# Optimization experiments

Measured on AMD Instinct MI355X. Metric: run time of the kernel, lower is better.

The kernel has to match this reference:

```python
import jax, jax.numpy as jnp
import numpy as np
from jax import lax

DT = 0.01        # self.dt
DT_SCALE = 1.0   # forward default


def _christoffel(v, x, U, W):
    # Low-rank quadratic Christoffel contraction (U, W as in verlet_fused):
    # gamma = (tanh(x @ U) * (v @ U)^2) @ W        [B, D]
    h = v @ U                 # [B, R]
    gate = jnp.tanh(x @ U)    # [B, R]
    return (gate * h * h) @ W


def setup_inputs() -> dict:
    key = jax.random.key(0)
    ks = jax.random.split(key, 5)
    B, D, R = 4096, 1024, 256
    x = jax.random.normal(ks[0], (B, D), dtype=jnp.float32)
    v = jax.random.normal(ks[1], (B, D), dtype=jnp.float32)
    force = jax.random.normal(ks[2], (B, D), dtype=jnp.float32)
    U = jax.random.normal(ks[3], (D, R), dtype=jnp.float32) * (D ** -0.5)
    W = jax.random.normal(ks[4], (R, D), dtype=jnp.float32) * (R ** -0.5)
    return {"x": x, "v": v, "force": force, "U": U, "W": W, "steps": 8}


def reference(x, v, force, U, W, steps):
    dt = jnp.float32(DT * DT_SCALE)
    half = jnp.float32(0.5)

    def step(carry, _):
        x, v = carry
        a = force - _christoffel(v, x, U, W)
        v_half = v + half * dt * a
        x = x + dt * v_half
        a_next = force - _christoffel(v_half, x, U, W)
        v = v_half + half * dt * a_next
        return (x, v), None

    (x, v), _ = lax.scan(step, (x, v), None, length=steps)
    return (x, v)
```

## Files before the change

kernel.cpp:

```cpp
#include <hip/hip_runtime.h>

typedef __bf16 bf16_t;
typedef __bf16 bf16x2 __attribute__((ext_vector_type(2)));
typedef __bf16 bf16x8 __attribute__((ext_vector_type(8)));
typedef float f32x4 __attribute__((ext_vector_type(4)));

#define MFMA_BF16(a, b, c) __builtin_amdgcn_mfma_f32_16x16x32_bf16((a), (b), (c), 0, 0, 0)

static constexpr int Bn = 4096;
static constexpr int Dn = 1024;
static constexpr int Rn = 256;
static constexpr int BT = 16;
static constexpr float DTv = 0.01f;
static constexpr float HDT = 0.005f;

__global__ void pack_u_kernel(const float* __restrict__ U, bf16_t* __restrict__ Upk) {
  int t = blockIdx.x * blockDim.x + threadIdx.x;
  int l = t & 63;
  int f = t >> 6;
  int kb = f & 31;
  int ct = f >> 5;
  int row0 = kb * 32 + (l >> 4) * 8;
  int col = ct * 16 + (l & 15);
  bf16x8 v;
#pragma unroll
  for (int j = 0; j < 8; ++j) v[j] = (bf16_t)U[(size_t)(row0 + j) * Rn + col];
  ((bf16x8*)Upk)[t] = v;
}

__global__ void pack_w_kernel(const float* __restrict__ W, bf16_t* __restrict__ Wpk) {
  int t = blockIdx.x * blockDim.x + threadIdx.x;
  int l = t & 63;
  int f = t >> 6;
  int kb = f & 7;
  int ct = f >> 3;
  int row0 = kb * 32 + (l >> 4) * 8;
  int col = ct * 16 + (l & 15);
  bf16x8 v;
#pragma unroll
  for (int j = 0; j < 8; ++j) v[j] = (bf16_t)W[(size_t)(row0 + j) * Dn + col];
  ((bf16x8*)Wpk)[t] = v;
}

__global__ __launch_bounds__(1024)
void wu_mfma_kernel(const float* __restrict__ W, const bf16_t* __restrict__ Upk,
                    bf16_t* __restrict__ WUpk) {
  __shared__ __align__(16) bf16_t wbuf[16 * 1032];
  const int tid = (int)threadIdx.x;
  const int wv = tid >> 6;
  const int l = tid & 63;
  const int ln = l & 15;
  const int quad = l >> 4;
  const int m = (int)blockIdx.x;
  {
    int row = tid >> 6;
    int c0 = (tid & 63) * 16;
    const float* src = W + (size_t)(m * 16 + row) * Dn + c0;
    bf16_t* dst = wbuf + row * 1032 + c0;
#pragma unroll
    for (int j = 0; j < 16; ++j) dst[j] = (bf16_t)src[j];
  }
  __syncthreads();
  f32x4 acc = {0.f, 0.f, 0.f, 0.f};
  const bf16x8* up = (const bf16x8*)Upk + (size_t)wv * 32 * 64 + l;
  const bf16_t* arow = wbuf + ln * 1032 + quad * 8;
  bf16x8 ur[4];
#pragma unroll
  for (int p = 0; p < 4; ++p) ur[p] = up[p * 64];
#pragma unroll
  for (int kb = 0; kb < 32; ++kb) {
    const bf16x8 a = *(const bf16x8*)(arow + kb * 32);
    const bf16x8 b = ur[kb & 3];
    if (kb < 28) ur[kb & 3] = up[(kb + 4) * 64];
    acc = MFMA_BF16(a, b, acc);
  }
#pragma unroll
  for (int r = 0; r < 4; ++r) {
    int rw = m * 16 + quad * 4 + r;
    int kb = rw >> 5;
    int sub = (rw >> 3) & 3;
    int j = rw & 7;
    size_t slot = ((size_t)(wv * 8 + kb) * 64 + sub * 16 + ln) * 8 + j;
    WUpk[slot] = (bf16_t)acc[r];
  }
}

__global__ __launch_bounds__(1024)
__attribute__((amdgpu_waves_per_eu(4, 4)))
void integrate_kernel(const float* __restrict__ x_in, const float* __restrict__ v_in,
                      const float* __restrict__ force,
                      const bf16_t* __restrict__ Upk, const bf16_t* __restrict__ Wpk,
                      const bf16_t* __restrict__ WUpk,
                      const int* __restrict__ steps_p, float* __restrict__ out) {
  __shared__ __align__(16) char smem[49920];
  bf16_t* abuf = (bf16_t*)smem;
  bf16_t* tbf = (bf16_t*)smem;
  bf16_t* sbuf = (bf16_t*)smem;

  const int tid = (int)threadIdx.x;
  const int wv = tid >> 6;
  const int l = tid & 63;
  const int ln = l & 15;
  const int quad = l >> 4;
  const int s = steps_p[0];
  const int nhalf = 2 * s;
  const int row_base = (int)blockIdx.x * BT;

  float* out_x = out;
  float* out_v = out + (size_t)Bn * Dn;

  float xs[4][4], vs[4][4];
  bf16x2 fs2[4][2];

#pragma unroll
  for (int i = 0; i < 4; ++i) {
    const int col = (wv * 4 + i) * 16 + ln;
#pragma unroll
    for (int r = 0; r < 4; ++r) {
      const size_t g = (size_t)(row_base + quad * 4 + r) * Dn + col;
      xs[i][r] = x_in[g];
      vs[i][r] = v_in[g];
      fs2[i][r >> 1][r & 1] = (bf16_t)force[g];
    }
  }

  f32x4 hx = {0.f, 0.f, 0.f, 0.f};
  f32x4 hv = {0.f, 0.f, 0.f, 0.f};
  f32x4 FU = {0.f, 0.f, 0.f, 0.f};
#pragma unroll
  for (int kh = 0; kh < 2; ++kh) {
    if ((wv >> 3) == kh) {
#pragma unroll
      for (int i = 0; i < 4; ++i) {
        const int col = (wv * 4 + i) * 16 + ln - kh * 512;
#pragma unroll
        for (int r = 0; r < 4; ++r) {
          const int ro = (quad * 4 + r) * 520 + col;
          abuf[ro] = (bf16_t)xs[i][r];
          abuf[8320 + ro] = (bf16_t)vs[i][r];
          abuf[16640 + ro] = fs2[i][r >> 1][r & 1];
        }
      }
    }
    __syncthreads();
    const bf16x8* up = (const bf16x8*)Upk + ((size_t)wv * 32 + kh * 16) * 64 + l;
    const bf16_t* ax = abuf + ln * 520 + quad * 8;
    bf16x8 ur[8];
#pragma unroll
    for (int p = 0; p < 8; ++p) ur[p] = up[p * 64];
#pragma unroll
    for (int kb = 0; kb < 16; ++kb) {
      const bf16x8 b = ur[kb & 7];
      if (kb < 8) ur[kb & 7] = up[(kb + 8) * 64];
      const bf16x8 a0 = *(const bf16x8*)(ax + kb * 32);
      const bf16x8 a1 = *(const bf16x8*)(ax + 8320 + kb * 32);
      const bf16x8 a2 = *(const bf16x8*)(ax + 16640 + kb * 32);
      hx = MFMA_BF16(a0, b, hx);
      hv = MFMA_BF16(a1, b, hv);
      FU = MFMA_BF16(a2, b, FU);
    }
    __syncthreads();
  }

  bf16x8 wu[8];
  {
    const bf16x8* wub = (const bf16x8*)WUpk + (size_t)wv * 8 * 64 + l;
#pragma unroll
    for (int kb = 0; kb < 8; ++kb) wu[kb] = wub[kb * 64];
  }

  f32x4 S1 = {0.f, 0.f, 0.f, 0.f};
  f32x4 S2 = {0.f, 0.f, 0.f, 0.f};
  for (int h = 0; h < nhalf; ++h) {
    if (h & 1) {
#pragma unroll
      for (int r = 0; r < 4; ++r) hx[r] += DTv * hv[r];
    }
    const float ch = (float)(s - ((h + 1) >> 1));
#pragma unroll
    for (int r = 0; r < 4; ++r) {
      float a = fminf(fmaxf(hx[r], -15.f), 15.f);
      const float e = __expf(2.f * a);
      const float gate = (e - 1.f) / (e + 1.f);
      const float t = gate * hv[r] * hv[r];
      S1[r] += t;
      S2[r] += ch * t;
      tbf[(quad * 4 + r) * 264 + wv * 16 + ln] = (bf16_t)t;
    }
    __syncthreads();
    f32x4 g = {0.f, 0.f, 0.f, 0.f};
    const bf16_t* trow = tbf + ln * 264 + quad * 8;
#pragma unroll
    for (int kb = 0; kb < 8; ++kb) {
      const bf16x8 a = *(const bf16x8*)(trow + kb * 32);
      g = MFMA_BF16(a, wu[kb], g);
    }
#pragma unroll
    for (int r = 0; r < 4; ++r) hv[r] += HDT * (FU[r] - g[r]);
    __syncthreads();
  }

#pragma unroll
  for (int r = 0; r < 4; ++r) {
    const int ro = (quad * 4 + r) * 264 + wv * 16 + ln;
    sbuf[ro] = (bf16_t)S1[r];
    sbuf[4224 + ro] = (bf16_t)S2[r];
  }
  __syncthreads();
  f32x4 ac1[4], ac2[4];
#pragma unroll
  for (int i = 0; i < 4; ++i) {
    ac1[i] = (f32x4){0.f, 0.f, 0.f, 0.f};
    ac2[i] = (f32x4){0.f, 0.f, 0.f, 0.f};
  }
  {
    const bf16x8* wp = (const bf16x8*)Wpk + (size_t)(wv * 4) * 8 * 64 + l;
    const bf16_t* s1row = sbuf + ln * 264 + quad * 8;
    const bf16_t* s2row = s1row + 4224;
    bf16x8 wr[4];
#pragma unroll
    for (int i = 0; i < 4; ++i) wr[i] = wp[i * 8 * 64];
#pragma unroll
    for (int kb = 0; kb < 8; ++kb) {
      const bf16x8 a1 = *(const bf16x8*)(s1row + kb * 32);
      const bf16x8 a2 = *(const bf16x8*)(s2row + kb * 32);
#pragma unroll
      for (int i = 0; i < 4; ++i) {
        const bf16x8 b = wr[i];
        if (kb < 7) wr[i] = wp[i * 8 * 64 + (kb + 1) * 64];
        ac1[i] = MFMA_BF16(a1, b, ac1[i]);
        ac2[i] = MFMA_BF16(a2, b, ac2[i]);
      }
    }
  }

  const float sf = (float)s;
  const float c_vf = sf * DTv;
  const float c_xf = sf * sf * DTv * HDT;
#pragma unroll
  for (int i = 0; i < 4; ++i) {
    const int col = (wv * 4 + i) * 16 + ln;
#pragma unroll
    for (int r = 0; r < 4; ++r) {
      const size_t g = (size_t)(row_base + quad * 4 + r) * Dn + col;
      const float fv = (float)fs2[i][r >> 1][r & 1];
      out_v[g] = vs[i][r] + c_vf * fv - HDT * ac1[i][r];
      out_x[g] = xs[i][r] + c_vf * vs[i][r] + c_xf * fv - DTv * HDT * ac2[i][r];
    }
  }
}

extern "C" void kernel_launch(void* const* d_in, const int* in_sizes, int n_in,
                              void* d_out, int out_size, void* d_ws, size_t ws_size,
                              hipStream_t stream) {
  const float* x = (const float*)d_in[0];
  const float* v = (const float*)d_in[1];
  const float* force = (const float*)d_in[2];
  const float* U = (const float*)d_in[3];
  const float* W = (const float*)d_in[4];
  const int* steps = (const int*)d_in[5];

  bf16_t* Upk = (bf16_t*)d_ws;
  bf16_t* Wpk = (bf16_t*)((char*)d_ws + 512 * 1024);
  bf16_t* WUpk = (bf16_t*)((char*)d_ws + 1024 * 1024);

  pack_u_kernel<<<128, 256, 0, stream>>>(U, Upk);
  pack_w_kernel<<<128, 256, 0, stream>>>(W, Wpk);
  wu_mfma_kernel<<<16, 1024, 0, stream>>>(W, Upk, WUpk);
  integrate_kernel<<<Bn / BT, 1024, 0, stream>>>(x, v, force, Upk, Wpk, WUpk, steps,
                                                 (float*)d_out);
}
```

Measured before the change: 165.4 us.

## Merge setup kernels, stage global I/O through swizzled LDS, double-buffer step scratch

The three setup kernels (pack U, pack W, W·U product) become one launch. The WU block now reads U directly from fp32 instead of waiting on the packed copy, so one launch boundary is gone. In the integrate kernel, the loads of x, v and force and the stores of both outputs go through a swizzled shared-memory transpose, giving coalesced 16-byte global accesses in place of scattered 4-byte ones. The per-step scratch buffer is double-buffered so one barrier per half-step can be dropped, and the W·U MFMA chain is split into two accumulators. These changes add barriers around each staged I/O chunk.

```diff
diff --git a/kernel.cpp b/kernel.cpp
--- a/kernel.cpp
+++ b/kernel.cpp
@@ -14,74 +14,79 @@
 static constexpr float DTv = 0.01f;
 static constexpr float HDT = 0.005f;
 
-__global__ void pack_u_kernel(const float* __restrict__ U, bf16_t* __restrict__ Upk) {
-  int t = blockIdx.x * blockDim.x + threadIdx.x;
-  int l = t & 63;
-  int f = t >> 6;
-  int kb = f & 31;
-  int ct = f >> 5;
-  int row0 = kb * 32 + (l >> 4) * 8;
-  int col = ct * 16 + (l & 15);
-  bf16x8 v;
-#pragma unroll
-  for (int j = 0; j < 8; ++j) v[j] = (bf16_t)U[(size_t)(row0 + j) * Rn + col];
-  ((bf16x8*)Upk)[t] = v;
-}
-
-__global__ void pack_w_kernel(const float* __restrict__ W, bf16_t* __restrict__ Wpk) {
-  int t = blockIdx.x * blockDim.x + threadIdx.x;
-  int l = t & 63;
-  int f = t >> 6;
-  int kb = f & 7;
-  int ct = f >> 3;
-  int row0 = kb * 32 + (l >> 4) * 8;
-  int col = ct * 16 + (l & 15);
-  bf16x8 v;
-#pragma unroll
-  for (int j = 0; j < 8; ++j) v[j] = (bf16_t)W[(size_t)(row0 + j) * Dn + col];
-  ((bf16x8*)Wpk)[t] = v;
-}
+__device__ __forceinline__ int swz(int col) { return col ^ (((col >> 5) & 7) << 2); }
 
 __global__ __launch_bounds__(1024)
-void wu_mfma_kernel(const float* __restrict__ W, const bf16_t* __restrict__ Upk,
-                    bf16_t* __restrict__ WUpk) {
+void setup_kernel(const float* __restrict__ U, const float* __restrict__ W,
+                  bf16_t* __restrict__ Upk, bf16_t* __restrict__ Wpk,
+                  bf16_t* __restrict__ WUpk) {
   __shared__ __align__(16) bf16_t wbuf[16 * 1032];
   const int tid = (int)threadIdx.x;
-  const int wv = tid >> 6;
-  const int l = tid & 63;
-  const int ln = l & 15;
-  const int quad = l >> 4;
-  const int m = (int)blockIdx.x;
-  {
-    int row = tid >> 6;
-    int c0 = (tid & 63) * 16;
-    const float* src = W + (size_t)(m * 16 + row) * Dn + c0;
-    bf16_t* dst = wbuf + row * 1032 + c0;
-#pragma unroll
-    for (int j = 0; j < 16; ++j) dst[j] = (bf16_t)src[j];
-  }
-  __syncthreads();
-  f32x4 acc = {0.f, 0.f, 0.f, 0.f};
-  const bf16x8* up = (const bf16x8*)Upk + (size_t)wv * 32 * 64 + l;
-  const bf16_t* arow = wbuf + ln * 1032 + quad * 8;
-  bf16x8 ur[4];
-#pragma unroll
-  for (int p = 0; p < 4; ++p) ur[p] = up[p * 64];
-#pragma unroll
-  for (int kb = 0; kb < 32; ++kb) {
-    const bf16x8 a = *(const bf16x8*)(arow + kb * 32);
-    const bf16x8 b = ur[kb & 3];
-    if (kb < 28) ur[kb & 3] = up[(kb + 4) * 64];
-    acc = MFMA_BF16(a, b, acc);
-  }
-#pragma unroll
-  for (int r = 0; r < 4; ++r) {
-    int rw = m * 16 + quad * 4 + r;
-    int kb = rw >> 5;
-    int sub = (rw >> 3) & 3;
-    int j = rw & 7;
-    size_t slot = ((size_t)(wv * 8 + kb) * 64 + sub * 16 + ln) * 8 + j;
-    WUpk[slot] = (bf16_t)acc[r];
+  const int b = (int)blockIdx.x;
+  if (b < 32) {
+    int t = b * 1024 + tid;
+    int l = t & 63, f = t >> 6;
+    int kb = f & 31, ct = f >> 5;
+    int row0 = kb * 32 + (l >> 4) * 8, col = ct * 16 + (l & 15);
+    bf16x8 v;
+#pragma unroll
+    for (int j = 0; j < 8; ++j) v[j] = (bf16_t)U[(size_t)(row0 + j) * Rn + col];
+    ((bf16x8*)Upk)[t] = v;
+  } else if (b < 64) {
+    int t = (b - 32) * 1024 + tid;
+    int l = t & 63, f = t >> 6;
+    int kb = f & 7, ct = f >> 3;
+    int row0 = kb * 32 + (l >> 4) * 8, col = ct * 16 + (l & 15);
+    bf16x8 v;
+#pragma unroll
+    for (int j = 0; j < 8; ++j) v[j] = (bf16_t)W[(size_t)(row0 + j) * Dn + col];
+    ((bf16x8*)Wpk)[t] = v;
+  } else {
+    const int m = b - 64;
+    const int wv = tid >> 6;
+    const int l = tid & 63;
+    const int ln = l & 15;
+    const int quad = l >> 4;
+    {
+      int row = tid >> 6;
+      int c0 = (tid & 63) * 16;
+      const float* src = W + (size_t)(m * 16 + row) * Dn + c0;
+      bf16_t* dst = wbuf + row * 1032 + c0;
+#pragma unroll
+      for (int j = 0; j < 16; ++j) dst[j] = (bf16_t)src[j];
+    }
+    __syncthreads();
+    const int ucol = wv * 16 + ln;
+    float uf[8][8];
+#pragma unroll
+    for (int p = 0; p < 8; ++p)
+#pragma unroll
+      for (int j = 0; j < 8; ++j)
+        uf[p][j] = U[(size_t)(p * 32 + quad * 8 + j) * Rn + ucol];
+    f32x4 acc = {0.f, 0.f, 0.f, 0.f};
+    const bf16_t* arow = wbuf + ln * 1032 + quad * 8;
+#pragma unroll
+    for (int kb = 0; kb < 32; ++kb) {
+      bf16x8 bb;
+#pragma unroll
+      for (int j = 0; j < 8; ++j) bb[j] = (bf16_t)uf[kb & 7][j];
+      const bf16x8 a = *(const bf16x8*)(arow + kb * 32);
+      acc = MFMA_BF16(a, bb, acc);
+      if (kb < 24) {
+#pragma unroll
+        for (int j = 0; j < 8; ++j)
+          uf[kb & 7][j] = U[(size_t)((kb + 8) * 32 + quad * 8 + j) * Rn + ucol];
+      }
+    }
+#pragma unroll
+    for (int r = 0; r < 4; ++r) {
+      int rw = m * 16 + quad * 4 + r;
+      int kb = rw >> 5;
+      int sub = (rw >> 3) & 3;
+      int j = rw & 7;
+      size_t slot = ((size_t)(wv * 8 + kb) * 64 + sub * 16 + ln) * 8 + j;
+      WUpk[slot] = (bf16_t)acc[r];
+    }
   }
 }
 
@@ -94,8 +99,7 @@
                       const int* __restrict__ steps_p, float* __restrict__ out) {
   __shared__ __align__(16) char smem[49920];
   bf16_t* abuf = (bf16_t*)smem;
-  bf16_t* tbf = (bf16_t*)smem;
-  bf16_t* sbuf = (bf16_t*)smem;
+  float* fsb = (float*)smem;
 
   const int tid = (int)threadIdx.x;
   const int wv = tid >> 6;
@@ -109,20 +113,39 @@
   float* out_x = out;
   float* out_v = out + (size_t)Bn * Dn;
 
+  const int frow = tid >> 7;
+  const int fr = (tid & 127) * 8;
+  const int sc0 = swz(fr);
+  const int sc1 = sc0 ^ 4;
+  int csw[4];
+#pragma unroll
+  for (int i = 0; i < 4; ++i) csw[i] = swz((wv * 4 + i) * 16 + ln);
+
   float xs[4][4], vs[4][4];
   bf16x2 fs2[4][2];
 
-#pragma unroll
-  for (int i = 0; i < 4; ++i) {
-    const int col = (wv * 4 + i) * 16 + ln;
-#pragma unroll
-    for (int r = 0; r < 4; ++r) {
-      const size_t g = (size_t)(row_base + quad * 4 + r) * Dn + col;
-      xs[i][r] = x_in[g];
-      vs[i][r] = v_in[g];
-      fs2[i][r >> 1][r & 1] = (bf16_t)force[g];
-    }
-  }
+  auto load_chunk = [&](const float* __restrict__ srcA, int HF, auto sink) {
+    const float* src_ = srcA + (size_t)(row_base + HF * 8) * Dn;
+    f32x4 a_ = *(const f32x4*)(src_ + tid * 8);
+    f32x4 b_ = *(const f32x4*)(src_ + tid * 8 + 4);
+    *(f32x4*)(fsb + frow * 1024 + sc0) = a_;
+    *(f32x4*)(fsb + frow * 1024 + sc1) = b_;
+    __syncthreads();
+    if ((quad >> 1) == HF) {
+#pragma unroll
+      for (int i = 0; i < 4; ++i)
+#pragma unroll
+        for (int r = 0; r < 4; ++r)
+          sink(i, r, fsb[((quad & 1) * 4 + r) * 1024 + csw[i]]);
+    }
+    __syncthreads();
+  };
+  load_chunk(x_in, 0, [&](int i, int r, float v_) { xs[i][r] = v_; });
+  load_chunk(x_in, 1, [&](int i, int r, float v_) { xs[i][r] = v_; });
+  load_chunk(v_in, 0, [&](int i, int r, float v_) { vs[i][r] = v_; });
+  load_chunk(v_in, 1, [&](int i, int r, float v_) { vs[i][r] = v_; });
+  load_chunk(force, 0, [&](int i, int r, float v_) { fs2[i][r >> 1][r & 1] = (bf16_t)v_; });
+  load_chunk(force, 1, [&](int i, int r, float v_) { fs2[i][r >> 1][r & 1] = (bf16_t)v_; });
 
   f32x4 hx = {0.f, 0.f, 0.f, 0.f};
   f32x4 hv = {0.f, 0.f, 0.f, 0.f};
@@ -171,12 +194,14 @@
 
   f32x4 S1 = {0.f, 0.f, 0.f, 0.f};
   f32x4 S2 = {0.f, 0.f, 0.f, 0.f};
+  bf16_t* tbase = (bf16_t*)smem;
   for (int h = 0; h < nhalf; ++h) {
     if (h & 1) {
 #pragma unroll
       for (int r = 0; r < 4; ++r) hx[r] += DTv * hv[r];
     }
     const float ch = (float)(s - ((h + 1) >> 1));
+    bf16_t* tb = tbase + (h & 1) * 4224;
 #pragma unroll
     for (int r = 0; r < 4; ++r) {
       float a = fminf(fmaxf(hx[r], -15.f), 15.f);
@@ -185,21 +210,23 @@
       const float t = gate * hv[r] * hv[r];
       S1[r] += t;
       S2[r] += ch * t;
-      tbf[(quad * 4 + r) * 264 + wv * 16 + ln] = (bf16_t)t;
-    }
-    __syncthreads();
-    f32x4 g = {0.f, 0.f, 0.f, 0.f};
-    const bf16_t* trow = tbf + ln * 264 + quad * 8;
-#pragma unroll
-    for (int kb = 0; kb < 8; ++kb) {
-      const bf16x8 a = *(const bf16x8*)(trow + kb * 32);
-      g = MFMA_BF16(a, wu[kb], g);
-    }
-#pragma unroll
-    for (int r = 0; r < 4; ++r) hv[r] += HDT * (FU[r] - g[r]);
-    __syncthreads();
-  }
-
+      tb[(quad * 4 + r) * 264 + wv * 16 + ln] = (bf16_t)t;
+    }
+    __syncthreads();
+    f32x4 g0 = {0.f, 0.f, 0.f, 0.f};
+    f32x4 g1 = {0.f, 0.f, 0.f, 0.f};
+    const bf16_t* trow = tb + ln * 264 + quad * 8;
+#pragma unroll
+    for (int kb = 0; kb < 8; kb += 2) {
+      g0 = MFMA_BF16(*(const bf16x8*)(trow + kb * 32), wu[kb], g0);
+      g1 = MFMA_BF16(*(const bf16x8*)(trow + (kb + 1) * 32), wu[kb + 1], g1);
+    }
+#pragma unroll
+    for (int r = 0; r < 4; ++r) hv[r] += HDT * (FU[r] - (g0[r] + g1[r]));
+  }
+  __syncthreads();
+
+  bf16_t* sbuf = (bf16_t*)smem;
 #pragma unroll
   for (int r = 0; r < 4; ++r) {
     const int ro = (quad * 4 + r) * 264 + wv * 16 + ln;
@@ -233,21 +260,36 @@
       }
     }
   }
+  __syncthreads();
 
   const float sf = (float)s;
   const float c_vf = sf * DTv;
   const float c_xf = sf * sf * DTv * HDT;
-#pragma unroll
-  for (int i = 0; i < 4; ++i) {
-    const int col = (wv * 4 + i) * 16 + ln;
-#pragma unroll
-    for (int r = 0; r < 4; ++r) {
-      const size_t g = (size_t)(row_base + quad * 4 + r) * Dn + col;
-      const float fv = (float)fs2[i][r >> 1][r & 1];
-      out_v[g] = vs[i][r] + c_vf * fv - HDT * ac1[i][r];
-      out_x[g] = xs[i][r] + c_vf * vs[i][r] + c_xf * fv - DTv * HDT * ac2[i][r];
-    }
-  }
+  auto store_chunk = [&](float* __restrict__ dstA, int HF, auto vex) {
+    if ((quad >> 1) == HF) {
+#pragma unroll
+      for (int i = 0; i < 4; ++i)
+#pragma unroll
+        for (int r = 0; r < 4; ++r)
+          fsb[((quad & 1) * 4 + r) * 1024 + csw[i]] = vex(i, r);
+    }
+    __syncthreads();
+    float* dst_ = dstA + (size_t)(row_base + HF * 8) * Dn;
+    *(f32x4*)(dst_ + tid * 8) = *(const f32x4*)(fsb + frow * 1024 + sc0);
+    *(f32x4*)(dst_ + tid * 8 + 4) = *(const f32x4*)(fsb + frow * 1024 + sc1);
+    __syncthreads();
+  };
+  auto vval = [&](int i, int r) {
+    return vs[i][r] + c_vf * (float)fs2[i][r >> 1][r & 1] - HDT * ac1[i][r];
+  };
+  auto xval = [&](int i, int r) {
+    return xs[i][r] + c_vf * vs[i][r] + c_xf * (float)fs2[i][r >> 1][r & 1] -
+           DTv * HDT * ac2[i][r];
+  };
+  store_chunk(out_v, 0, vval);
+  store_chunk(out_v, 1, vval);
+  store_chunk(out_x, 0, xval);
+  store_chunk(out_x, 1, xval);
 }
 
 extern "C" void kernel_launch(void* const* d_in, const int* in_sizes, int n_in,
@@ -264,9 +306,7 @@
   bf16_t* Wpk = (bf16_t*)((char*)d_ws + 512 * 1024);
   bf16_t* WUpk = (bf16_t*)((char*)d_ws + 1024 * 1024);
 
-  pack_u_kernel<<<128, 256, 0, stream>>>(U, Upk);
-  pack_w_kernel<<<128, 256, 0, stream>>>(W, Wpk);
-  wu_mfma_kernel<<<16, 1024, 0, stream>>>(W, Upk, WUpk);
+  setup_kernel<<<80, 1024, 0, stream>>>(U, W, Upk, Wpk, WUpk);
   integrate_kernel<<<Bn / BT, 1024, 0, stream>>>(x, v, force, Upk, Wpk, WUpk, steps,
                                                  (float*)d_out);
 }
```

Result: faster. 159.9 us (-3.4%).
